# Optimization experiments

Measured on AMD Instinct MI355X. Metric: run time of the kernel, lower is better.

The kernel has to match this reference:

```python
import jax, jax.numpy as jnp
import numpy as np

PAD_ID = 0    # scibert [PAD]
SEP_ID = 103  # scibert [SEP]
IGNORE = 100


def setup_inputs() -> dict:
    key = jax.random.key(0)
    ks = jax.random.split(key, 8)
    B, S, D, T = 64, 512, 768, 2
    return {
        "sequence_output": jax.random.normal(ks[0], (B, S, D), dtype=jnp.float32),
        "input_ids": jax.random.randint(ks[1], (B, S), 0, 31090, dtype=jnp.int64),
        "labels": jax.random.randint(ks[2], (B, S), 0, 2, dtype=jnp.int64),
        "W": jax.random.normal(ks[3], (T, D), dtype=jnp.float32) * 0.02,
        "b": jax.random.normal(ks[4], (T,), dtype=jnp.float32) * 0.02,
        "start_trans": jax.random.normal(ks[5], (T,), dtype=jnp.float32) * 0.1,
        "end_trans": jax.random.normal(ks[6], (T,), dtype=jnp.float32) * 0.1,
        "trans": jax.random.normal(ks[7], (T, T), dtype=jnp.float32) * 0.1,
    }


def _crf_llh_token_mean(em, tags, start, end, trans):
    # em: [B,S,T], tags: [B,S]; mask=None in torchcrf => all-ones mask.
    B, S, T = em.shape
    # numerator: score of the gold path
    em_tag = jnp.take_along_axis(em, tags[..., None], axis=2)[..., 0]        # [B,S]
    tr_tag = trans[tags[:, :-1], tags[:, 1:]]                                 # [B,S-1]
    score = start[tags[:, 0]] + em_tag.sum(1) + tr_tag.sum(1) + end[tags[:, -1]]
    # denominator: forward algorithm over time (scan over S-1 tiny steps)
    alpha0 = start[None, :] + em[:, 0]                                        # [B,T]
    em_rest = jnp.swapaxes(em[:, 1:], 0, 1)                                   # [S-1,B,T]

    def step(alpha, em_t):
        # alpha[b,i] + trans[i,j] + em_t[b,j] -> logsumexp over i
        nxt = jax.nn.logsumexp(alpha[:, :, None] + trans[None], axis=1) + em_t
        return nxt, None

    alpha, _ = jax.lax.scan(step, alpha0, em_rest)
    logZ = jax.nn.logsumexp(alpha + end[None, :], axis=1)                     # [B]
    llh = score - logZ
    # reduction='token_mean' with all-ones mask -> sum / (B*S)
    return llh.sum() / jnp.float32(B * S)


def _crf_viterbi(em, start, end, trans):
    # em: [B,S,T] -> decoded tags [B,S] int32
    B, S, T = em.shape
    score0 = start[None, :] + em[:, 0]                                        # [B,T]
    em_rest = jnp.swapaxes(em[:, 1:], 0, 1)                                   # [S-1,B,T]

    def vstep(score, em_t):
        cand = score[:, :, None] + trans[None] + em_t[:, None, :]             # [B,T,T]
        return cand.max(axis=1), cand.argmax(axis=1).astype(jnp.int32)

    final, hist = jax.lax.scan(vstep, score0, em_rest)                        # hist [S-1,B,T]
    final = final + end[None, :]
    last = jnp.argmax(final, axis=1).astype(jnp.int32)                        # [B]

    def back(tag, bp_t):
        prev = jnp.take_along_axis(bp_t, tag[:, None], axis=1)[:, 0]
        return prev, prev

    _, prevs = jax.lax.scan(back, last, hist, reverse=True)                   # [S-1,B]
    tags = jnp.concatenate([prevs, last[None, :]], axis=0)                    # [S,B]
    return jnp.swapaxes(tags, 0, 1)                                           # [B,S]


def reference(sequence_output, input_ids, labels, W, b, start_trans, end_trans, trans):
    mask = (input_ids != PAD_ID) & (input_ids != SEP_ID) & (labels != IGNORE)  # [B,S] bool
    seq = sequence_output * mask[..., None].astype(sequence_output.dtype)
    labels_m = labels * mask.astype(labels.dtype)
    # probablities = relu(hidden2tag(seq))
    em = jax.nn.relu(jnp.einsum("bsd,td->bst", seq, W) + b)                    # [B,S,2]
    loss = _crf_llh_token_mean(em, labels_m, start_trans, end_trans, trans)
    target_emissions = _crf_viterbi(em, start_trans, end_trans, trans).astype(jnp.float32)
    return (loss, target_emissions, labels_m, mask)
```

## Files before the change

### kernel.cpp

```cpp
#include <hip/hip_runtime.h>

#define BB 64
#define SS 512
#define DD 768
#define NROWS (BB*SS)
#define NEG (-1e30f)
#define NCH 16
#define CL  32

__global__ __launch_bounds__(256) void k_emissions(
    const float* __restrict__ seq,
    const int*   __restrict__ input_ids,
    const int*   __restrict__ labels,
    const float* __restrict__ W,
    const float* __restrict__ bias,
    float* __restrict__ em_t,
    int*   __restrict__ tags_t,
    float* __restrict__ out)
{
    const int lane = threadIdx.x & 63;
    const int wid  = blockIdx.x * 4 + (threadIdx.x >> 6);
    const int base = wid * 4;

    const float4* W4 = (const float4*)W;
    float4 w0[3], w1[3];
#pragma unroll
    for (int j = 0; j < 3; ++j) {
        w0[j] = W4[j*64 + lane];
        w1[j] = W4[192 + j*64 + lane];
    }
    const float b0 = bias[0], b1 = bias[1];

    const float4* s4 = (const float4*)seq;
    float4 v[4][3];
#pragma unroll
    for (int r = 0; r < 4; ++r)
#pragma unroll
        for (int j = 0; j < 3; ++j)
            v[r][j] = s4[(size_t)(base + r)*192 + j*64 + lane];

    float d0[4], d1[4];
#pragma unroll
    for (int r = 0; r < 4; ++r) {
        float a0 = 0.f, a1 = 0.f;
#pragma unroll
        for (int j = 0; j < 3; ++j) {
            float4 x = v[r][j];
            a0 += x.x*w0[j].x + x.y*w0[j].y + x.z*w0[j].z + x.w*w0[j].w;
            a1 += x.x*w1[j].x + x.y*w1[j].y + x.z*w1[j].z + x.w*w1[j].w;
        }
        d0[r] = a0; d1[r] = a1;
    }
#pragma unroll
    for (int m = 32; m >= 1; m >>= 1) {
#pragma unroll
        for (int r = 0; r < 4; ++r) {
            d0[r] += __shfl_xor(d0[r], m, 64);
            d1[r] += __shfl_xor(d1[r], m, 64);
        }
    }
    if (lane < 4) {
        const float dd0 = (lane==0) ? d0[0] : (lane==1) ? d0[1] : (lane==2) ? d0[2] : d0[3];
        const float dd1 = (lane==0) ? d1[0] : (lane==1) ? d1[1] : (lane==2) ? d1[2] : d1[3];
        const int row = base + lane;
        const int id  = input_ids[row];
        const int lab = labels[row];
        const int msk = (id != 0 && id != 103 && lab != 100) ? 1 : 0;
        const int lm  = lab * msk;
        const float e0 = fmaxf((msk ? dd0 : 0.f) + b0, 0.f);
        const float e1 = fmaxf((msk ? dd1 : 0.f) + b1, 0.f);
        const int b_ = row >> 9, s_ = row & 511;
        *(float2*)(em_t + (s_*BB + b_)*2) = make_float2(e0, e1);
        tags_t[s_*BB + b_] = lm;
        out[1 + NROWS   + row] = (float)lm;
        out[1 + 2*NROWS + row] = (float)msk;
    }
}

__device__ __forceinline__ float lse2(float x, float y) {
    float m = fmaxf(x, y);
    float d = fminf(x, y) - m;
    return m + __logf(1.f + __expf(d));
}

#define STEP_LE(e_, g_) do { \
    float Ex = __expf((e_).x), Ey = __expf((e_).y); \
    float B00 = X00*Ex, B10 = X10*Ex, B01 = X01*Ey, B11 = X11*Ey; \
    float n00 = fmaf(p00, B00, p01*B10); \
    float n01 = fmaf(p00, B01, p01*B11); \
    float n10 = fmaf(p10, B00, p11*B10); \
    float n11 = fmaf(p10, B01, p11*B11); \
    p00 = n00; p01 = n01; p10 = n10; p11 = n11; \
    score += (ptag ? ((g_) ? t11 : t10) : ((g_) ? t01 : t00)) \
           + ((g_) ? (e_).y : (e_).x); \
    ptag = (g_); \
} while (0)

#define RENORM() do { \
    float m0 = fmaxf(p00, p01), m1 = fmaxf(p10, p11); \
    float r0 = __builtin_amdgcn_rcpf(m0), r1 = __builtin_amdgcn_rcpf(m1); \
    p00 *= r0; p01 *= r0; p10 *= r1; p11 *= r1; \
    lc0 += __logf(m0); lc1 += __logf(m1); \
} while (0)

#define STEP_VP(e_) do { \
    float n0 = fmaxf(V00 + t00, V01 + t10) + (e_).x; \
    float n1 = fmaxf(V00 + t01, V01 + t11) + (e_).y; \
    float n2 = fmaxf(V10 + t00, V11 + t10) + (e_).x; \
    float n3 = fmaxf(V10 + t01, V11 + t11) + (e_).y; \
    V00 = n0; V01 = n1; V10 = n2; V11 = n3; \
} while (0)

#define STEP_BPF(i_, e_) do { \
    float c00 = v0 + t00, c10 = v1 + t10; \
    float c01 = v0 + t01, c11 = v1 + t11; \
    int bp0 = (c10 > c00); int bp1 = (c11 > c01); \
    v0 = fmaxf(c00, c10) + (e_).x; v1 = fmaxf(c01, c11) + (e_).y; \
    unsigned two = (unsigned)(bp0 | (bp1 << 1)); \
    if ((i_) < 16) w0 |= two << (2*(i_)); else w1 |= two << (2*((i_)-16)); \
    int nF0 = bp0 ? F1 : F0; int nF1 = bp1 ? F1 : F0; \
    F0 = nF0; F1 = nF1; \
} while (0)

__global__ __launch_bounds__(128, 1) void k_crf1(
    const float* __restrict__ em_t,
    const int*   __restrict__ tags_t,
    const float* __restrict__ start,
    const float* __restrict__ trans,
    float* __restrict__ logP4g,
    float* __restrict__ scoreg,
    float* __restrict__ vitP4g)
{
    const int b  = threadIdx.x & 63;
    const int c  = blockIdx.x;
    const int k0 = c * CL;
    const float t00 = trans[0], t01 = trans[1], t10 = trans[2], t11 = trans[3];
    const float2* em2 = (const float2*)em_t;

    if (threadIdx.x < 64) {
        const float s0 = start[0], s1 = start[1];
        const float X00 = __expf(t00), X01 = __expf(t01),
                    X10 = __expf(t10), X11 = __expf(t11);
        float2 e[32]; int g[32];
#pragma unroll
        for (int i = 0; i < 32; ++i) {
            e[i] = em2[(k0+i)*BB + b];
            g[i] = tags_t[(k0+i)*BB + b];
        }
        float p00, p01, p10, p11, lc0 = 0.f, lc1 = 0.f, score;
        int ptag;
        if (c == 0) {
            p00 = 1.f; p01 = 0.f; p10 = 0.f; p11 = 1.f;
            score = g[0] ? (s1 + e[0].y) : (s0 + e[0].x);
        } else {
            int pt = tags_t[(k0-1)*BB + b];
            float Ex = __expf(e[0].x), Ey = __expf(e[0].y);
            p00 = X00*Ex; p01 = X01*Ey; p10 = X10*Ex; p11 = X11*Ey;
            score = (pt ? (g[0] ? t11 : t10) : (g[0] ? t01 : t00))
                  + (g[0] ? e[0].y : e[0].x);
        }
        ptag = g[0];
#pragma unroll
        for (int i = 1; i < 32; ++i) {
            STEP_LE(e[i], g[i]);
            if ((i & 7) == 7) RENORM();
        }
        float4 P = make_float4(fmaxf(__logf(p00) + lc0, NEG),
                               fmaxf(__logf(p01) + lc0, NEG),
                               fmaxf(__logf(p10) + lc1, NEG),
                               fmaxf(__logf(p11) + lc1, NEG));
        ((float4*)logP4g)[c*BB + b] = P;
        scoreg[c*BB + b] = score;
    } else {
        float2 e[32];
#pragma unroll
        for (int i = 0; i < 32; ++i) e[i] = em2[(k0+i)*BB + b];
        float V00, V01, V10, V11;
        if (c == 0) {
            V00 = 0.f; V01 = NEG; V10 = NEG; V11 = 0.f;
        } else {
            V00 = t00 + e[0].x; V01 = t01 + e[0].y;
            V10 = t10 + e[0].x; V11 = t11 + e[0].y;
        }
#pragma unroll
        for (int i = 1; i < 32; ++i) STEP_VP(e[i]);
        ((float4*)vitP4g)[c*BB + b] = make_float4(V00, V01, V10, V11);
    }
}

__global__ __launch_bounds__(1024) void k_crf2(
    const float* __restrict__ em_t,
    const int*   __restrict__ tags_t,
    const float* __restrict__ start,
    const float* __restrict__ endt,
    const float* __restrict__ trans,
    const float* __restrict__ logP4g,
    const float* __restrict__ scoreg,
    const float* __restrict__ vitP4g,
    float* __restrict__ out)
{
    __shared__ float2 vbound[NCH][BB];
    __shared__ unsigned char Fsh[NCH][BB];
    __shared__ int lastSh[BB];
    __shared__ unsigned int tagbits[BB*17];

    const int tid = threadIdx.x;
    const int b   = tid & 63;
    const int c   = tid >> 6;
    const int k0  = c * CL;
    const float t00 = trans[0], t01 = trans[1], t10 = trans[2], t11 = trans[3];
    const float s0 = start[0], s1 = start[1];
    const float en0 = endt[0], en1 = endt[1];
    const float2* em2 = (const float2*)em_t;

    if (blockIdx.x == 0) {
        if (c == 0) {
            float2 em0v = em2[b];
            float a0 = s0 + em0v.x, a1 = s1 + em0v.y, sc = 0.f;
#pragma unroll
            for (int cc = 0; cc < NCH; ++cc) {
                float4 P = ((const float4*)logP4g)[cc*BB + b];
                float n0 = lse2(a0 + P.x, a1 + P.z);
                float n1 = lse2(a0 + P.y, a1 + P.w);
                a0 = n0; a1 = n1;
                sc += scoreg[cc*BB + b];
            }
            int tagL = tags_t[511*BB + b];
            sc += tagL ? en1 : en0;
            float logZ = lse2(a0 + en0, a1 + en1);
            float llh = sc - logZ;
#pragma unroll
            for (int m = 32; m >= 1; m >>= 1) llh += __shfl_xor(llh, m, 64);
            if (b == 0) out[0] = llh / (float)NROWS;
        }
    } else {
        if (c == 0) {
            float2 em0v = em2[b];
            float v0 = s0 + em0v.x, v1 = s1 + em0v.y;
            vbound[0][b] = make_float2(v0, v1);
#pragma unroll
            for (int cc = 0; cc < NCH; ++cc) {
                float4 V = ((const float4*)vitP4g)[cc*BB + b];
                float n0 = fmaxf(v0 + V.x, v1 + V.z);
                float n1 = fmaxf(v0 + V.y, v1 + V.w);
                v0 = n0; v1 = n1;
                if (cc < NCH-1) vbound[cc+1][b] = make_float2(v0, v1);
            }
            lastSh[b] = (v1 + en1 > v0 + en0) ? 1 : 0;
        }
        __syncthreads();

        unsigned w0 = 0u, w1 = 0u;
        int F0 = 0, F1 = 1;
        {
            float2 vb = vbound[c][b];
            float v0 = vb.x, v1 = vb.y;
            float2 e[8];
#pragma unroll
            for (int i = 0; i < 8; ++i) e[i] = em2[(k0+i)*BB + b];
            if (c != 0) STEP_BPF(0, e[0]);
#pragma unroll
            for (int i = 1; i < 8; ++i) STEP_BPF(i, e[i]);
#pragma unroll
            for (int j = 1; j < 4; ++j) {
#pragma unroll
                for (int i = 0; i < 8; ++i) e[i] = em2[(k0 + j*8 + i)*BB + b];
#pragma unroll
                for (int i = 0; i < 8; ++i) STEP_BPF(j*8 + i, e[i]);
            }
        }
        Fsh[c][b] = (unsigned char)(F0 | (F1 << 1));
        __syncthreads();

        {
            int t = lastSh[b];
            for (int cc = NCH-1; cc > c; --cc)
                t = (Fsh[cc][b] >> t) & 1;
            unsigned word = ((unsigned)t) << 31;
#pragma unroll
            for (int i = 31; i >= 1; --i) {
                unsigned pair = ((i >= 16) ? (w1 >> (2*(i-16)))
                                           : (w0 >> (2*i))) & 3u;
                t = (int)((pair >> t) & 1u);
                word |= ((unsigned)t) << (i - 1);
            }
            tagbits[b*17 + c] = word;
        }
        __syncthreads();

        for (int idx = tid; idx < NROWS; idx += 1024) {
            const int bq = idx >> 9, k = idx & 511;
            unsigned wd = tagbits[bq*17 + (k >> 5)];
            out[1 + idx] = (float)((wd >> (k & 31)) & 1);
        }
    }
}

extern "C" void kernel_launch(void* const* d_in, const int* in_sizes, int n_in,
                              void* d_out, int out_size, void* d_ws, size_t ws_size,
                              hipStream_t stream) {
    const float* seq    = (const float*)d_in[0];
    const int*   ids    = (const int*)  d_in[1];
    const int*   labels = (const int*)  d_in[2];
    const float* W      = (const float*)d_in[3];
    const float* bias   = (const float*)d_in[4];
    const float* start  = (const float*)d_in[5];
    const float* endt   = (const float*)d_in[6];
    const float* trans  = (const float*)d_in[7];
    float* out = (float*)d_out;

    float* em_t   = (float*)d_ws;
    int*   tags_t = (int*)  ((char*)d_ws + (size_t) 65536*4);
    float* logP4g = (float*)((char*)d_ws + (size_t) 98304*4);
    float* scoreg = (float*)((char*)d_ws + (size_t)102400*4);
    float* vitP4g = (float*)((char*)d_ws + (size_t)103424*4);

    k_emissions<<<2048, 256, 0, stream>>>(seq, ids, labels, W, bias, em_t, tags_t, out);
    k_crf1<<<16, 128, 0, stream>>>(em_t, tags_t, start, trans, logP4g, scoreg, vitP4g);
    k_crf2<<<2, 1024, 0, stream>>>(em_t, tags_t, start, endt, trans,
                                   logP4g, scoreg, vitP4g, out);
}
```

Before: 172.2 us.

## Merge CRF kernels into one grid-barrier kernel and reshape emission dot product

The two CRF kernels become one 16-block kernel that uses two software grid barriers (atomic counters reset by the emissions kernel). Emissions stay in registers across phases, and each block writes its own chunk of Viterbi output, replacing the serialized 2-block tail kernel. The emissions kernel now gives each row 16 lanes with a 4-step shuffle reduction instead of a full-wave reduction per row. This removes a kernel launch and the single-block serial tail, but the barrier assumes all 16 blocks are co-resident and adds atomic spin-wait latency.

```diff
diff --git a/kernel.cpp b/kernel.cpp
--- a/kernel.cpp
+++ b/kernel.cpp
@@ -16,59 +16,41 @@
     const float* __restrict__ bias,
     float* __restrict__ em_t,
     int*   __restrict__ tags_t,
+    unsigned* __restrict__ ctrs,
     float* __restrict__ out)
 {
+    if (blockIdx.x == 0 && threadIdx.x < 2) ctrs[threadIdx.x] = 0u;
+
     const int lane = threadIdx.x & 63;
+    const int l    = lane & 15;
+    const int rr   = lane >> 4;
     const int wid  = blockIdx.x * 4 + (threadIdx.x >> 6);
-    const int base = wid * 4;
+    const int row  = wid * 4 + rr;
 
     const float4* W4 = (const float4*)W;
-    float4 w0[3], w1[3];
-#pragma unroll
-    for (int j = 0; j < 3; ++j) {
-        w0[j] = W4[j*64 + lane];
-        w1[j] = W4[192 + j*64 + lane];
-    }
-    const float b0 = bias[0], b1 = bias[1];
-
-    const float4* s4 = (const float4*)seq;
-    float4 v[4][3];
-#pragma unroll
-    for (int r = 0; r < 4; ++r)
-#pragma unroll
-        for (int j = 0; j < 3; ++j)
-            v[r][j] = s4[(size_t)(base + r)*192 + j*64 + lane];
-
-    float d0[4], d1[4];
-#pragma unroll
-    for (int r = 0; r < 4; ++r) {
-        float a0 = 0.f, a1 = 0.f;
-#pragma unroll
-        for (int j = 0; j < 3; ++j) {
-            float4 x = v[r][j];
-            a0 += x.x*w0[j].x + x.y*w0[j].y + x.z*w0[j].z + x.w*w0[j].w;
-            a1 += x.x*w1[j].x + x.y*w1[j].y + x.z*w1[j].z + x.w*w1[j].w;
-        }
-        d0[r] = a0; d1[r] = a1;
-    }
-#pragma unroll
-    for (int m = 32; m >= 1; m >>= 1) {
-#pragma unroll
-        for (int r = 0; r < 4; ++r) {
-            d0[r] += __shfl_xor(d0[r], m, 64);
-            d1[r] += __shfl_xor(d1[r], m, 64);
-        }
-    }
-    if (lane < 4) {
-        const float dd0 = (lane==0) ? d0[0] : (lane==1) ? d0[1] : (lane==2) ? d0[2] : d0[3];
-        const float dd1 = (lane==0) ? d1[0] : (lane==1) ? d1[1] : (lane==2) ? d1[2] : d1[3];
-        const int row = base + lane;
+    const float4* s4 = (const float4*)seq + (size_t)row * 192;
+
+    float a0 = 0.f, a1 = 0.f;
+#pragma unroll
+    for (int j = 0; j < 12; ++j) {
+        float4 x  = s4[j*16 + l];
+        float4 w0 = W4[j*16 + l];
+        float4 w1 = W4[192 + j*16 + l];
+        a0 += x.x*w0.x + x.y*w0.y + x.z*w0.z + x.w*w0.w;
+        a1 += x.x*w1.x + x.y*w1.y + x.z*w1.z + x.w*w1.w;
+    }
+#pragma unroll
+    for (int m = 8; m >= 1; m >>= 1) {
+        a0 += __shfl_xor(a0, m, 64);
+        a1 += __shfl_xor(a1, m, 64);
+    }
+    if (l == 0) {
         const int id  = input_ids[row];
         const int lab = labels[row];
         const int msk = (id != 0 && id != 103 && lab != 100) ? 1 : 0;
         const int lm  = lab * msk;
-        const float e0 = fmaxf((msk ? dd0 : 0.f) + b0, 0.f);
-        const float e1 = fmaxf((msk ? dd1 : 0.f) + b1, 0.f);
+        const float e0 = fmaxf((msk ? a0 : 0.f) + bias[0], 0.f);
+        const float e1 = fmaxf((msk ? a1 : 0.f) + bias[1], 0.f);
         const int b_ = row >> 9, s_ = row & 511;
         *(float2*)(em_t + (s_*BB + b_)*2) = make_float2(e0, e1);
         tags_t[s_*BB + b_] = lm;
@@ -122,47 +104,72 @@
     F0 = nF0; F1 = nF1; \
 } while (0)
 
-__global__ __launch_bounds__(128, 1) void k_crf1(
+__device__ __forceinline__ void grid_barrier(unsigned* cnt) {
+    __syncthreads();
+    if (threadIdx.x == 0) {
+        __threadfence();
+        __hip_atomic_fetch_add(cnt, 1u, __ATOMIC_ACQ_REL, __HIP_MEMORY_SCOPE_AGENT);
+        while (__hip_atomic_load(cnt, __ATOMIC_ACQUIRE, __HIP_MEMORY_SCOPE_AGENT) < 16u) {
+            __builtin_amdgcn_s_sleep(2);
+        }
+    }
+    __syncthreads();
+}
+
+__global__ __launch_bounds__(128, 1) void k_crf(
     const float* __restrict__ em_t,
     const int*   __restrict__ tags_t,
     const float* __restrict__ start,
+    const float* __restrict__ endt,
     const float* __restrict__ trans,
     float* __restrict__ logP4g,
     float* __restrict__ scoreg,
-    float* __restrict__ vitP4g)
+    float* __restrict__ vitP4g,
+    unsigned char* __restrict__ Fg,
+    unsigned* __restrict__ ctrs,
+    float* __restrict__ out)
 {
+    __shared__ unsigned int wordSh[BB];
+
     const int b  = threadIdx.x & 63;
     const int c  = blockIdx.x;
     const int k0 = c * CL;
     const float t00 = trans[0], t01 = trans[1], t10 = trans[2], t11 = trans[3];
+    const float s0 = start[0], s1 = start[1];
+    const float en0 = endt[0], en1 = endt[1];
     const float2* em2 = (const float2*)em_t;
 
+    float2 e[32];
+    float mvb0 = 0.f, mvb1 = 0.f;
+    int last = 0;
+    unsigned w0 = 0u, w1 = 0u;
+    int F0 = 0, F1 = 1;
+
     if (threadIdx.x < 64) {
-        const float s0 = start[0], s1 = start[1];
         const float X00 = __expf(t00), X01 = __expf(t01),
                     X10 = __expf(t10), X11 = __expf(t11);
-        float2 e[32]; int g[32];
+        float2 le[32]; int g[32];
 #pragma unroll
         for (int i = 0; i < 32; ++i) {
-            e[i] = em2[(k0+i)*BB + b];
-            g[i] = tags_t[(k0+i)*BB + b];
+            le[i] = em2[(k0+i)*BB + b];
+            g[i]  = tags_t[(k0+i)*BB + b];
         }
         float p00, p01, p10, p11, lc0 = 0.f, lc1 = 0.f, score;
         int ptag;
         if (c == 0) {
             p00 = 1.f; p01 = 0.f; p10 = 0.f; p11 = 1.f;
-            score = g[0] ? (s1 + e[0].y) : (s0 + e[0].x);
+            score = g[0] ? (s1 + le[0].y) : (s0 + le[0].x);
         } else {
             int pt = tags_t[(k0-1)*BB + b];
-            float Ex = __expf(e[0].x), Ey = __expf(e[0].y);
+            float Ex = __expf(le[0].x), Ey = __expf(le[0].y);
             p00 = X00*Ex; p01 = X01*Ey; p10 = X10*Ex; p11 = X11*Ey;
             score = (pt ? (g[0] ? t11 : t10) : (g[0] ? t01 : t00))
-                  + (g[0] ? e[0].y : e[0].x);
+                  + (g[0] ? le[0].y : le[0].x);
         }
         ptag = g[0];
 #pragma unroll
         for (int i = 1; i < 32; ++i) {
-            STEP_LE(e[i], g[i]);
+            STEP_LE(le[i], g[i]);
             if ((i & 7) == 7) RENORM();
         }
         float4 P = make_float4(fmaxf(__logf(p00) + lc0, NEG),
@@ -172,7 +179,6 @@
         ((float4*)logP4g)[c*BB + b] = P;
         scoreg[c*BB + b] = score;
     } else {
-        float2 e[32];
 #pragma unroll
         for (int i = 0; i < 32; ++i) e[i] = em2[(k0+i)*BB + b];
         float V00, V01, V10, V11;
@@ -186,34 +192,9 @@
         for (int i = 1; i < 32; ++i) STEP_VP(e[i]);
         ((float4*)vitP4g)[c*BB + b] = make_float4(V00, V01, V10, V11);
     }
-}
-
-__global__ __launch_bounds__(1024) void k_crf2(
-    const float* __restrict__ em_t,
-    const int*   __restrict__ tags_t,
-    const float* __restrict__ start,
-    const float* __restrict__ endt,
-    const float* __restrict__ trans,
-    const float* __restrict__ logP4g,
-    const float* __restrict__ scoreg,
-    const float* __restrict__ vitP4g,
-    float* __restrict__ out)
-{
-    __shared__ float2 vbound[NCH][BB];
-    __shared__ unsigned char Fsh[NCH][BB];
-    __shared__ int lastSh[BB];
-    __shared__ unsigned int tagbits[BB*17];
-
-    const int tid = threadIdx.x;
-    const int b   = tid & 63;
-    const int c   = tid >> 6;
-    const int k0  = c * CL;
-    const float t00 = trans[0], t01 = trans[1], t10 = trans[2], t11 = trans[3];
-    const float s0 = start[0], s1 = start[1];
-    const float en0 = endt[0], en1 = endt[1];
-    const float2* em2 = (const float2*)em_t;
-
-    if (blockIdx.x == 0) {
+    grid_barrier(&ctrs[0]);
+
+    if (threadIdx.x < 64) {
         if (c == 0) {
             float2 em0v = em2[b];
             float a0 = s0 + em0v.x, a1 = s1 + em0v.y, sc = 0.f;
@@ -234,64 +215,55 @@
             if (b == 0) out[0] = llh / (float)NROWS;
         }
     } else {
-        if (c == 0) {
-            float2 em0v = em2[b];
-            float v0 = s0 + em0v.x, v1 = s1 + em0v.y;
-            vbound[0][b] = make_float2(v0, v1);
-#pragma unroll
-            for (int cc = 0; cc < NCH; ++cc) {
-                float4 V = ((const float4*)vitP4g)[cc*BB + b];
-                float n0 = fmaxf(v0 + V.x, v1 + V.z);
-                float n1 = fmaxf(v0 + V.y, v1 + V.w);
-                v0 = n0; v1 = n1;
-                if (cc < NCH-1) vbound[cc+1][b] = make_float2(v0, v1);
-            }
-            lastSh[b] = (v1 + en1 > v0 + en0) ? 1 : 0;
-        }
-        __syncthreads();
-
-        unsigned w0 = 0u, w1 = 0u;
-        int F0 = 0, F1 = 1;
+        float2 em0v = em2[b];
+        float v0 = s0 + em0v.x, v1 = s1 + em0v.y;
+        mvb0 = v0; mvb1 = v1;
+#pragma unroll
+        for (int cc = 0; cc < NCH; ++cc) {
+            if (cc == c) { mvb0 = v0; mvb1 = v1; }
+            float4 V = ((const float4*)vitP4g)[cc*BB + b];
+            float n0 = fmaxf(v0 + V.x, v1 + V.z);
+            float n1 = fmaxf(v0 + V.y, v1 + V.w);
+            v0 = n0; v1 = n1;
+        }
+        last = (v1 + en1 > v0 + en0) ? 1 : 0;
+
         {
-            float2 vb = vbound[c][b];
-            float v0 = vb.x, v1 = vb.y;
-            float2 e[8];
-#pragma unroll
-            for (int i = 0; i < 8; ++i) e[i] = em2[(k0+i)*BB + b];
+            float v0b = mvb0, v1b = mvb1;
+            float v0 = v0b, v1 = v1b;
             if (c != 0) STEP_BPF(0, e[0]);
 #pragma unroll
-            for (int i = 1; i < 8; ++i) STEP_BPF(i, e[i]);
-#pragma unroll
-            for (int j = 1; j < 4; ++j) {
-#pragma unroll
-                for (int i = 0; i < 8; ++i) e[i] = em2[(k0 + j*8 + i)*BB + b];
-#pragma unroll
-                for (int i = 0; i < 8; ++i) STEP_BPF(j*8 + i, e[i]);
-            }
-        }
-        Fsh[c][b] = (unsigned char)(F0 | (F1 << 1));
-        __syncthreads();
-
-        {
-            int t = lastSh[b];
-            for (int cc = NCH-1; cc > c; --cc)
-                t = (Fsh[cc][b] >> t) & 1;
-            unsigned word = ((unsigned)t) << 31;
-#pragma unroll
-            for (int i = 31; i >= 1; --i) {
-                unsigned pair = ((i >= 16) ? (w1 >> (2*(i-16)))
-                                           : (w0 >> (2*i))) & 3u;
-                t = (int)((pair >> t) & 1u);
-                word |= ((unsigned)t) << (i - 1);
-            }
-            tagbits[b*17 + c] = word;
-        }
-        __syncthreads();
-
-        for (int idx = tid; idx < NROWS; idx += 1024) {
-            const int bq = idx >> 9, k = idx & 511;
-            unsigned wd = tagbits[bq*17 + (k >> 5)];
-            out[1 + idx] = (float)((wd >> (k & 31)) & 1);
+            for (int i = 1; i < 32; ++i) STEP_BPF(i, e[i]);
+        }
+        Fg[c*BB + b] = (unsigned char)(F0 | (F1 << 1));
+    }
+    grid_barrier(&ctrs[1]);
+
+    if (threadIdx.x >= 64) {
+        int t = last;
+#pragma unroll
+        for (int cc = NCH-1; cc >= 1; --cc) {
+            unsigned f = (unsigned)Fg[cc*BB + b];
+            int tn = (int)((f >> t) & 1u);
+            t = (cc > c) ? tn : t;
+        }
+        unsigned word = ((unsigned)t) << 31;
+#pragma unroll
+        for (int i = 31; i >= 1; --i) {
+            unsigned pair = ((i >= 16) ? (w1 >> (2*(i-16)))
+                                       : (w0 >> (2*i))) & 3u;
+            t = (int)((pair >> t) & 1u);
+            word |= ((unsigned)t) << (i - 1);
+        }
+        wordSh[b] = word;
+    }
+    __syncthreads();
+
+    {
+        const int sl = threadIdx.x & 31;
+        for (int bb = (threadIdx.x >> 5); bb < BB; bb += 4) {
+            unsigned wd = wordSh[bb];
+            out[1 + bb*SS + k0 + sl] = (float)((wd >> sl) & 1u);
         }
     }
 }
@@ -309,14 +281,16 @@
     const float* trans  = (const float*)d_in[7];
     float* out = (float*)d_out;
 
-    float* em_t   = (float*)d_ws;
-    int*   tags_t = (int*)  ((char*)d_ws + (size_t) 65536*4);
-    float* logP4g = (float*)((char*)d_ws + (size_t) 98304*4);
-    float* scoreg = (float*)((char*)d_ws + (size_t)102400*4);
-    float* vitP4g = (float*)((char*)d_ws + (size_t)103424*4);
-
-    k_emissions<<<2048, 256, 0, stream>>>(seq, ids, labels, W, bias, em_t, tags_t, out);
-    k_crf1<<<16, 128, 0, stream>>>(em_t, tags_t, start, trans, logP4g, scoreg, vitP4g);
-    k_crf2<<<2, 1024, 0, stream>>>(em_t, tags_t, start, endt, trans,
-                                   logP4g, scoreg, vitP4g, out);
-}
+    float*         em_t   = (float*)d_ws;
+    int*           tags_t = (int*)   ((char*)d_ws + (size_t) 65536*4);
+    float*         logP4g = (float*) ((char*)d_ws + (size_t) 98304*4);
+    float*         scoreg = (float*) ((char*)d_ws + (size_t)102400*4);
+    float*         vitP4g = (float*) ((char*)d_ws + (size_t)103424*4);
+    unsigned char* Fg     = (unsigned char*)((char*)d_ws + (size_t)107520*4);
+    unsigned*      ctrs   = (unsigned*)((char*)d_ws + (size_t)107776*4);
+
+    k_emissions<<<2048, 256, 0, stream>>>(seq, ids, labels, W, bias,
+                                          em_t, tags_t, ctrs, out);
+    k_crf<<<16, 128, 0, stream>>>(em_t, tags_t, start, endt, trans,
+                                  logP4g, scoreg, vitP4g, Fg, ctrs, out);
+}
```

Result: no change. 174.3 us (+1.2%).
